# Performance work log

Hardware: AMD Instinct MI355X
Metric: run time of the kernel (lower is better)

## Reference

```python
import jax, jax.numpy as jnp
import numpy as np
import math

D_MODEL = 1024
HEADS = 16
D_K = D_MODEL // HEADS
BATCH = 4
SEQ = 1024


def setup_inputs() -> dict:
    key = jax.random.key(0)
    ks = jax.random.split(key, 12)
    s = 1.0 / math.sqrt(D_MODEL)
    inp = {
        "q": jax.random.normal(ks[0], (BATCH, SEQ, D_MODEL), jnp.float32),
        "k": jax.random.normal(ks[1], (BATCH, SEQ, D_MODEL), jnp.float32),
        "v": jax.random.normal(ks[2], (BATCH, SEQ, D_MODEL), jnp.float32),
        # causal mask, broadcastable over (batch, heads)
        "mask": jnp.tril(jnp.ones((SEQ, SEQ), jnp.bool_))[None, None, :, :],
        "Wq": jax.random.normal(ks[3], (D_MODEL, D_MODEL), jnp.float32) * s,
        "bq": jax.random.normal(ks[4], (D_MODEL,), jnp.float32) * 0.01,
        "Wk": jax.random.normal(ks[5], (D_MODEL, D_MODEL), jnp.float32) * s,
        "bk": jax.random.normal(ks[6], (D_MODEL,), jnp.float32) * 0.01,
        "Wv": jax.random.normal(ks[7], (D_MODEL, D_MODEL), jnp.float32) * s,
        "bv": jax.random.normal(ks[8], (D_MODEL,), jnp.float32) * 0.01,
        "Wo": jax.random.normal(ks[9], (D_MODEL, D_MODEL), jnp.float32) * s,
        "bo": jax.random.normal(ks[10], (D_MODEL,), jnp.float32) * 0.01,
    }
    return inp


def reference(q, k, v, mask, Wq, bq, Wk, bk, Wv, bv, Wo, bo):
    B, S, _ = q.shape
    # projections (torch Linear: x @ W.T + b; here W stored as [in, out])
    def proj(x, W, b):
        return (x @ W + b).reshape(B, -1, HEADS, D_K).transpose(0, 2, 1, 3)

    Q = proj(q, Wq, bq)  # [B, H, S, Dk]
    K = proj(k, Wk, bk)
    V = proj(v, Wv, bv)

    scores = jnp.einsum("bhqd,bhkd->bhqk", Q, K) / math.sqrt(D_K)
    scores = jnp.where(mask, scores, jnp.float32(-1e9))
    attn = jax.nn.softmax(scores, axis=-1)  # dropout p=0.0 -> identity
    x = jnp.einsum("bhqk,bhkd->bhqd", attn, V)
    x = x.transpose(0, 2, 1, 3).reshape(B, S, D_MODEL)
    return x @ Wo + bo
```

## Files before the change

kernel.cpp:

```cpp
#include <hip/hip_runtime.h>
#include <math.h>

typedef __bf16 bf16_t;
typedef bf16_t bf16x8 __attribute__((ext_vector_type(8)));
typedef bf16_t bf16x4 __attribute__((ext_vector_type(4)));
typedef float  floatx4 __attribute__((ext_vector_type(4)));
typedef unsigned int u32;

#define MFMA_BF16(a, b, c) __builtin_amdgcn_mfma_f32_16x16x32_bf16((a), (b), (c), 0, 0, 0)

static constexpr int DMODEL = 1024;
static constexpr int NHEAD  = 16;
static constexpr int HDIM   = 64;
static constexpr int NBATCH = 4;
static constexpr int SEQLEN = 1024;
static constexpr int NTOK   = NBATCH * SEQLEN;

typedef __attribute__((address_space(3))) void       as3_void;
typedef __attribute__((address_space(1))) const void as1_cvoid;

__device__ __forceinline__ void gload16(const void* g, void* l) {
    __builtin_amdgcn_global_load_lds((as1_cvoid*)g, (as3_void*)l, 16, 0, 0);
}

__device__ __forceinline__ bf16x8 load_cvt8(const float* __restrict__ p) {
    floatx4 a = *(const floatx4*)p;
    floatx4 b = *(const floatx4*)(p + 4);
    bf16x8 r;
    r[0] = (bf16_t)a[0]; r[1] = (bf16_t)a[1]; r[2] = (bf16_t)a[2]; r[3] = (bf16_t)a[3];
    r[4] = (bf16_t)b[0]; r[5] = (bf16_t)b[1]; r[6] = (bf16_t)b[2]; r[7] = (bf16_t)b[3];
    return r;
}

__global__ __launch_bounds__(256) void prep(
    const float* __restrict__ W0, const float* __restrict__ W1,
    const float* __restrict__ W2, const float* __restrict__ W3,
    const float* __restrict__ q, const float* __restrict__ k, const float* __restrict__ v,
    bf16_t* __restrict__ Wt, bf16_t* __restrict__ Xr)
{
    __shared__ float tile[32][33];
    const int z = blockIdx.z;
    if (z < 4) {
        const float* W = (z == 0) ? W0 : (z == 1) ? W1 : (z == 2) ? W2 : W3;
        bf16_t* O = Wt + (size_t)z * DMODEL * DMODEL;
        const int tx = threadIdx.x & 31, ty = threadIdx.x >> 5;
        const int r0 = blockIdx.x * 32, c0 = blockIdx.y * 32;
#pragma unroll
        for (int i = 0; i < 32; i += 8)
            tile[ty + i][tx] = W[(size_t)(r0 + ty + i) * DMODEL + c0 + tx];
        __syncthreads();
#pragma unroll
        for (int i = 0; i < 32; i += 8)
            O[(size_t)(c0 + ty + i) * DMODEL + r0 + tx] = (bf16_t)tile[tx][ty + i];
    } else {
        const float* src = (z == 4) ? q : (z == 5) ? k : v;
        bf16_t* dst = Xr + (size_t)(z - 4) * ((size_t)NTOK * DMODEL);
        size_t i = (((size_t)blockIdx.y * 32 + blockIdx.x) * 256 + threadIdx.x) * 16;
        *(bf16x8*)(dst + i)     = load_cvt8(src + i);
        *(bf16x8*)(dst + i + 8) = load_cvt8(src + i + 8);
    }
}

__global__ __launch_bounds__(256) void transpose_w(
    const float* __restrict__ W0, const float* __restrict__ W1,
    const float* __restrict__ W2, const float* __restrict__ W3,
    bf16_t* __restrict__ out)
{
    __shared__ float tile[32][33];
    const float* W = (blockIdx.z == 0) ? W0 : (blockIdx.z == 1) ? W1
                   : (blockIdx.z == 2) ? W2 : W3;
    bf16_t* O = out + (size_t)blockIdx.z * DMODEL * DMODEL;
    int tx = threadIdx.x, ty = threadIdx.y;
    int r0 = blockIdx.x * 32, c0 = blockIdx.y * 32;
#pragma unroll
    for (int i = 0; i < 32; i += 8)
        tile[ty + i][tx] = W[(size_t)(r0 + ty + i) * DMODEL + c0 + tx];
    __syncthreads();
#pragma unroll
    for (int i = 0; i < 32; i += 8)
        O[(size_t)(c0 + ty + i) * DMODEL + r0 + tx] = (bf16_t)tile[tx][ty + i];
}
__global__ __launch_bounds__(256) void cvt_bf16(
    const float* __restrict__ src, bf16_t* __restrict__ dst)
{
    size_t i = ((size_t)blockIdx.x * 256 + threadIdx.x) * 8;
    *(bf16x8*)(dst + i) = load_cvt8(src + i);
}

__global__ __launch_bounds__(256) void gemm_qkv(
    const bf16_t* __restrict__ Xb, size_t astride, int mode0,
    const bf16_t* __restrict__ Wt,
    const float* __restrict__ bq, const float* __restrict__ bk, const float* __restrict__ bv,
    bf16_t* __restrict__ Qh, bf16_t* __restrict__ Kh, bf16_t* __restrict__ Vt)
{
    const int mode = mode0 + blockIdx.z;
    const bf16_t* A = Xb + astride * (size_t)blockIdx.z;
    const bf16_t* B = Wt + (size_t)mode * DMODEL * DMODEL;
    const float* bias = (mode == 0) ? bq : (mode == 1) ? bk : bv;
    bf16_t* out       = (mode == 0) ? Qh : (mode == 1) ? Kh : Vt;

    __shared__ __align__(16) bf16_t lA[2][128 * 32];
    __shared__ __align__(16) bf16_t lB[2][128 * 32];

    const int wave = threadIdx.x >> 6, lane = threadIdx.x & 63;
    const int quad = lane >> 4, l15 = lane & 15;
    const int wm = wave >> 1, wn = wave & 1;
    const int row0 = blockIdx.x * 128, col0 = blockIdx.y * 128;
    const int srow = lane >> 2, scol = (lane & 3) * 8;

    const floatx4 zero = {0.f, 0.f, 0.f, 0.f};
    floatx4 acc[4][4];
#pragma unroll
    for (int mt = 0; mt < 4; mt++)
#pragma unroll
        for (int nt = 0; nt < 4; nt++) acc[mt][nt] = zero;

#pragma unroll
    for (int j = 0; j < 2; j++) {
        const int seg = j * 4 + wave;
        gload16(A + (size_t)(row0 + seg * 16 + srow) * DMODEL + scol, lA[0] + seg * 512);
        gload16(B + (size_t)(col0 + seg * 16 + srow) * DMODEL + scol, lB[0] + seg * 512);
    }

    for (int it = 0; it < 32; it++) {
        __syncthreads();
        const int cur = it & 1;
        if (it + 1 < 32) {
            const int k1 = (it + 1) * 32;
            const int nb = cur ^ 1;
#pragma unroll
            for (int j = 0; j < 2; j++) {
                const int seg = j * 4 + wave;
                gload16(A + (size_t)(row0 + seg * 16 + srow) * DMODEL + k1 + scol, lA[nb] + seg * 512);
                gload16(B + (size_t)(col0 + seg * 16 + srow) * DMODEL + k1 + scol, lB[nb] + seg * 512);
            }
        }
        bf16x8 aF[4], bF[4];
#pragma unroll
        for (int t = 0; t < 4; t++) {
            aF[t] = *(const bf16x8*)(lA[cur] + (wm * 64 + t * 16 + l15) * 32 + quad * 8);
            bF[t] = *(const bf16x8*)(lB[cur] + (wn * 64 + t * 16 + l15) * 32 + quad * 8);
        }
#pragma unroll
        for (int mt = 0; mt < 4; mt++)
#pragma unroll
            for (int nt = 0; nt < 4; nt++)
                acc[mt][nt] = MFMA_BF16(aF[mt], bF[nt], acc[mt][nt]);
    }

#pragma unroll
    for (int nt = 0; nt < 4; nt++) {
        const int gn = col0 + wn * 64 + nt * 16 + l15;
        const float bb = bias[gn];
        const int hh = gn >> 6, dd = gn & 63;
#pragma unroll
        for (int mt = 0; mt < 4; mt++) {
#pragma unroll
            for (int r = 0; r < 4; r++) {
                const int tok = row0 + wm * 64 + mt * 16 + quad * 4 + r;
                const int b = tok >> 10, s = tok & 1023;
                float vv = acc[mt][nt][r] + bb;
                size_t addr;
                if (mode == 2) {
                    addr = ((size_t)((b * NHEAD + hh) * HDIM + dd)) * SEQLEN + s;
                } else {
                    if (mode == 0) vv *= 0.125f;
                    addr = ((size_t)((b * NHEAD + hh) * SEQLEN + s)) * HDIM + dd;
                }
                out[addr] = (bf16_t)vv;
            }
        }
    }
}

__global__ __launch_bounds__(256) void gemm_o(
    const bf16_t* __restrict__ Xa, const bf16_t* __restrict__ Wt,
    const float* __restrict__ bias, float* __restrict__ out)
{
    __shared__ __align__(16) bf16_t lA[2][64 * 32];
    __shared__ __align__(16) bf16_t lB[2][128 * 32];

    const int wave = threadIdx.x >> 6, lane = threadIdx.x & 63;
    const int quad = lane >> 4, l15 = lane & 15;
    const int wm = wave & 1, wn = wave >> 1;
    const int row0 = blockIdx.x * 64, col0 = blockIdx.y * 128;
    const int srow = lane >> 2, scol = (lane & 3) * 8;

    const floatx4 zero = {0.f, 0.f, 0.f, 0.f};
    floatx4 acc[2][4];
#pragma unroll
    for (int mt = 0; mt < 2; mt++)
#pragma unroll
        for (int nt = 0; nt < 4; nt++) acc[mt][nt] = zero;

    gload16(Xa + (size_t)(row0 + wave * 16 + srow) * DMODEL + scol, lA[0] + wave * 512);
#pragma unroll
    for (int j = 0; j < 2; j++) {
        const int seg = wave * 2 + j;
        gload16(Wt + (size_t)(col0 + seg * 16 + srow) * DMODEL + scol, lB[0] + seg * 512);
    }

    for (int it = 0; it < 32; it++) {
        __syncthreads();
        const int cur = it & 1;
        if (it + 1 < 32) {
            const int k1 = (it + 1) * 32;
            const int nb = cur ^ 1;
            gload16(Xa + (size_t)(row0 + wave * 16 + srow) * DMODEL + k1 + scol, lA[nb] + wave * 512);
#pragma unroll
            for (int j = 0; j < 2; j++) {
                const int seg = wave * 2 + j;
                gload16(Wt + (size_t)(col0 + seg * 16 + srow) * DMODEL + k1 + scol, lB[nb] + seg * 512);
            }
        }
        bf16x8 aF[2], bF[4];
#pragma unroll
        for (int t = 0; t < 2; t++)
            aF[t] = *(const bf16x8*)(lA[cur] + (wm * 32 + t * 16 + l15) * 32 + quad * 8);
#pragma unroll
        for (int t = 0; t < 4; t++)
            bF[t] = *(const bf16x8*)(lB[cur] + (wn * 64 + t * 16 + l15) * 32 + quad * 8);
#pragma unroll
        for (int mt = 0; mt < 2; mt++)
#pragma unroll
            for (int nt = 0; nt < 4; nt++)
                acc[mt][nt] = MFMA_BF16(aF[mt], bF[nt], acc[mt][nt]);
    }

#pragma unroll
    for (int nt = 0; nt < 4; nt++) {
        const int gn = col0 + wn * 64 + nt * 16 + l15;
        const float bb = bias[gn];
#pragma unroll
        for (int mt = 0; mt < 2; mt++) {
#pragma unroll
            for (int r = 0; r < 4; r++) {
                const int tok = row0 + wm * 32 + mt * 16 + quad * 4 + r;
                out[(size_t)tok * DMODEL + gn] = acc[mt][nt][r] + bb;
            }
        }
    }
}

#define SOFTMAX_PV(S0x, S1x, qbase, qrow, lacc, oacc) do {                             \
    const bool nomask = (kb + 31 <= (qbase));                                          \
    float ps = 0.f;                                                                    \
    union { bf16_t hh2[8]; u32 u[4]; } pk;                                             \
    _Pragma("unroll") for (int r = 0; r < 4; r++) {                                    \
        const int key0 = kb + quad * 4 + r;                                            \
        float s0 = (nomask || key0 <= (qrow))      ? S0x[r] : -1e30f;                  \
        float s1 = (nomask || key0 + 16 <= (qrow)) ? S1x[r] : -1e30f;                  \
        float e0 = __expf(s0), e1 = __expf(s1);                                        \
        ps += e0 + e1;                                                                 \
        pk.hh2[r] = (bf16_t)e0; pk.hh2[4 + r] = (bf16_t)e1;                            \
    }                                                                                  \
    lacc += ps;                                                                        \
    u32 a0 = __shfl(pk.u[0], srcA), a1 = __shfl(pk.u[1], srcA);                        \
    u32 a2 = __shfl(pk.u[0], srcB), a3 = __shfl(pk.u[1], srcB);                        \
    u32 b0 = __shfl(pk.u[2], srcA), b1 = __shfl(pk.u[3], srcA);                        \
    u32 b2 = __shfl(pk.u[2], srcB), b3 = __shfl(pk.u[3], srcB);                        \
    union { u32 u[4]; bf16x8 v; } bP;                                                  \
    bP.u[0] = hiP ? b0 : a0; bP.u[1] = hiP ? b1 : a1;                                  \
    bP.u[2] = hiP ? b2 : a2; bP.u[3] = hiP ? b3 : a3;                                  \
    _Pragma("unroll") for (int dt = 0; dt < 4; dt++)                                   \
        oacc[dt] = MFMA_BF16(Vv[dt], bP.v, oacc[dt]);                                  \
} while (0)

__global__ __launch_bounds__(256, 4) void attn(
    const bf16_t* __restrict__ Qh, const bf16_t* __restrict__ Kh,
    const bf16_t* __restrict__ Vt, bf16_t* __restrict__ X)
{
    __shared__ __align__(8) float comb[2][64][34];
    const int wave = threadIdx.x >> 6, lane = threadIdx.x & 63;
    const int quad = lane >> 4, l15 = lane & 15;
    const int L = blockIdx.x;
    const int bh = (L & 7) * 8 + ((L >> 3) & 7);
    const int t  = L >> 6;
    const int b = bh >> 4, h = bh & 15;

    const int qbaseA = 16 * t, qbaseB = 1008 - 16 * t;
    const int qrowA = qbaseA + l15, qrowB = qbaseB + l15;
    const int nkA = t / 2 + 1, nkB = 32 - t / 2;

    const bf16_t* Qp = Qh + (size_t)bh * SEQLEN * HDIM;
    const bf16_t* Kp = Kh + (size_t)bh * SEQLEN * HDIM;
    const bf16_t* Vp = Vt + (size_t)bh * HDIM * SEQLEN;

    bf16x8 bQA[2], bQB[2];
#pragma unroll
    for (int c = 0; c < 2; c++) {
        bQA[c] = *(const bf16x8*)(Qp + (size_t)qrowA * HDIM + c * 32 + quad * 8);
        bQB[c] = *(const bf16x8*)(Qp + (size_t)qrowB * HDIM + c * 32 + quad * 8);
    }

    const floatx4 zero = {0.f, 0.f, 0.f, 0.f};
    float lA_ = 0.f, lB_ = 0.f;
    floatx4 oA[4], oB[4];
#pragma unroll
    for (int dt = 0; dt < 4; dt++) { oA[dt] = zero; oB[dt] = zero; }

    const int srcA = ((quad & 1) ? 32 : 0) + l15;
    const int srcB = srcA + 16;
    const bool hiP = (quad >= 2);

    for (int kc = wave; kc < nkB; kc += 4) {
        const int kb = kc * 32;
        bf16x8 K0[2], K1[2], Vv[4];
#pragma unroll
        for (int c = 0; c < 2; c++) {
            K0[c] = *(const bf16x8*)(Kp + (size_t)(kb + l15) * HDIM + c * 32 + quad * 8);
            K1[c] = *(const bf16x8*)(Kp + (size_t)(kb + 16 + l15) * HDIM + c * 32 + quad * 8);
        }
#pragma unroll
        for (int dt = 0; dt < 4; dt++)
            Vv[dt] = *(const bf16x8*)(Vp + (size_t)(dt * 16 + l15) * SEQLEN + kb + quad * 8);

        const bool doA = (kc < nkA);
        floatx4 S0B = zero, S1B = zero, S0A = zero, S1A = zero;
#pragma unroll
        for (int c = 0; c < 2; c++) {
            S0B = MFMA_BF16(K0[c], bQB[c], S0B);
            S1B = MFMA_BF16(K1[c], bQB[c], S1B);
        }
        if (doA) {
#pragma unroll
            for (int c = 0; c < 2; c++) {
                S0A = MFMA_BF16(K0[c], bQA[c], S0A);
                S1A = MFMA_BF16(K1[c], bQA[c], S1A);
            }
        }
        SOFTMAX_PV(S0B, S1B, qbaseB, qrowB, lB_, oB);
        if (doA) { SOFTMAX_PV(S0A, S1A, qbaseA, qrowA, lA_, oA); }
    }

    auto publish = [&](int slot) {
        float2* d2 = (float2*)&comb[slot][lane][0];
#pragma unroll
        for (int dt = 0; dt < 4; dt++) {
            d2[2 * dt]     = make_float2(oA[dt][0], oA[dt][1]);
            d2[2 * dt + 1] = make_float2(oA[dt][2], oA[dt][3]);
            d2[8 + 2 * dt]     = make_float2(oB[dt][0], oB[dt][1]);
            d2[8 + 2 * dt + 1] = make_float2(oB[dt][2], oB[dt][3]);
        }
        d2[16] = make_float2(lA_, lB_);
    };
    auto accum = [&](int slot) {
        const float2* s2 = (const float2*)&comb[slot][lane][0];
#pragma unroll
        for (int dt = 0; dt < 4; dt++) {
            float2 x0 = s2[2 * dt], x1 = s2[2 * dt + 1];
            float2 y0 = s2[8 + 2 * dt], y1 = s2[8 + 2 * dt + 1];
            oA[dt][0] += x0.x; oA[dt][1] += x0.y; oA[dt][2] += x1.x; oA[dt][3] += x1.y;
            oB[dt][0] += y0.x; oB[dt][1] += y0.y; oB[dt][2] += y1.x; oB[dt][3] += y1.y;
        }
        float2 lp = s2[16];
        lA_ += lp.x; lB_ += lp.y;
    };

    if (wave & 1) publish(wave >> 1);
    __syncthreads();
    if (!(wave & 1)) accum(wave >> 1);
    __syncthreads();
    if (wave == 2) publish(0);
    __syncthreads();
    if (wave == 0) {
        accum(0);

        lA_ += __shfl_xor(lA_, 16); lA_ += __shfl_xor(lA_, 32);
        lB_ += __shfl_xor(lB_, 16); lB_ += __shfl_xor(lB_, 32);

        const float invA = 1.f / lA_, invB = 1.f / lB_;
#pragma unroll
        for (int dt = 0; dt < 4; dt++) {
            bf16x4 va, vb;
#pragma unroll
            for (int r = 0; r < 4; r++) {
                va[r] = (bf16_t)(oA[dt][r] * invA);
                vb[r] = (bf16_t)(oB[dt][r] * invB);
            }
            const size_t cofs = (size_t)h * HDIM + dt * 16 + quad * 4;
            *(bf16x4*)(&X[((size_t)(b * SEQLEN + qrowA)) * DMODEL + cofs]) = va;
            *(bf16x4*)(&X[((size_t)(b * SEQLEN + qrowB)) * DMODEL + cofs]) = vb;
        }
    }
}

extern "C" void kernel_launch(void* const* d_in, const int* in_sizes, int n_in,
                              void* d_out, int out_size, void* d_ws, size_t ws_size,
                              hipStream_t stream)
{
    const float* q  = (const float*)d_in[0];
    const float* k  = (const float*)d_in[1];
    const float* v  = (const float*)d_in[2];
    const float* Wq = (const float*)d_in[4];
    const float* bq = (const float*)d_in[5];
    const float* Wk = (const float*)d_in[6];
    const float* bk = (const float*)d_in[7];
    const float* Wv = (const float*)d_in[8];
    const float* bv = (const float*)d_in[9];
    const float* Wo = (const float*)d_in[10];
    const float* bo = (const float*)d_in[11];
    float* out = (float*)d_out;

    char* ws = (char*)d_ws;
    const size_t MB = 1ull << 20;
    const size_t NELEM = (size_t)NTOK * DMODEL;
    bf16_t* Wt = (bf16_t*)ws;
    bf16_t* Qh = (bf16_t*)(ws + 8 * MB);
    bf16_t* Kh = (bf16_t*)(ws + 16 * MB);
    bf16_t* Vt = (bf16_t*)(ws + 24 * MB);
    bf16_t* Xr = (bf16_t*)(ws + 32 * MB);

    if (ws_size >= 56 * MB) {
        prep<<<dim3(32, 32, 7), dim3(256), 0, stream>>>(Wq, Wk, Wv, Wo, q, k, v, Wt, Xr);
        gemm_qkv<<<dim3(32, 8, 3), dim3(256), 0, stream>>>(
            Xr, NELEM, 0, Wt, bq, bk, bv, Qh, Kh, Vt);
    } else {
        transpose_w<<<dim3(32, 32, 4), dim3(32, 8), 0, stream>>>(Wq, Wk, Wv, Wo, Wt);
        const float* qkv_in[3] = {q, k, v};
        for (int m = 0; m < 3; m++) {
            cvt_bf16<<<dim3(2048), dim3(256), 0, stream>>>(qkv_in[m], Xr);
            gemm_qkv<<<dim3(32, 8, 1), dim3(256), 0, stream>>>(
                Xr, 0, m, Wt, bq, bk, bv, Qh, Kh, Vt);
        }
    }

    bf16_t* Xa = Xr;
    attn<<<dim3(2048), dim3(256), 0, stream>>>(Qh, Kh, Vt, Xa);
    gemm_o<<<dim3(64, 8), dim3(256), 0, stream>>>(
        Xa, Wt + 3 * (size_t)DMODEL * DMODEL, bo, out);
}
```

Measured before the change: 238.0 us.

## Double-buffer K/V loads in attention loop, use exp2 with folded log2e scale

Restructures the attention key loop into a two-stage software pipeline: the next K/V chunk is loaded into registers while the current one is computed, with sched_barriers keeping the loads ahead of the compute. Folds log2(e) into the Q scale so softmax can call a native exp2, and splits the fully unmasked path from the masked one to skip per-element mask checks. Raises MFMA wave priority and lowers launch bounds occupancy from 4 to 2 to make room for the extra registers held by the double buffers.

```diff
diff --git a/kernel.cpp b/kernel.cpp
--- a/kernel.cpp
+++ b/kernel.cpp
@@ -8,6 +8,12 @@
 typedef unsigned int u32;
 
 #define MFMA_BF16(a, b, c) __builtin_amdgcn_mfma_f32_16x16x32_bf16((a), (b), (c), 0, 0, 0)
+
+#if __has_builtin(__builtin_amdgcn_exp2f)
+#define EXP2F(x) __builtin_amdgcn_exp2f(x)
+#else
+#define EXP2F(x) exp2f(x)
+#endif
 
 static constexpr int DMODEL = 1024;
 static constexpr int NHEAD  = 16;
@@ -164,7 +170,7 @@
                 if (mode == 2) {
                     addr = ((size_t)((b * NHEAD + hh) * HDIM + dd)) * SEQLEN + s;
                 } else {
-                    if (mode == 0) vv *= 0.125f;
+                    if (mode == 0) vv *= 0.1803368801111204f;
                     addr = ((size_t)((b * NHEAD + hh) * SEQLEN + s)) * HDIM + dd;
                 }
                 out[addr] = (bf16_t)vv;
@@ -242,19 +248,7 @@
     }
 }
 
-#define SOFTMAX_PV(S0x, S1x, qbase, qrow, lacc, oacc) do {                             \
-    const bool nomask = (kb + 31 <= (qbase));                                          \
-    float ps = 0.f;                                                                    \
-    union { bf16_t hh2[8]; u32 u[4]; } pk;                                             \
-    _Pragma("unroll") for (int r = 0; r < 4; r++) {                                    \
-        const int key0 = kb + quad * 4 + r;                                            \
-        float s0 = (nomask || key0 <= (qrow))      ? S0x[r] : -1e30f;                  \
-        float s1 = (nomask || key0 + 16 <= (qrow)) ? S1x[r] : -1e30f;                  \
-        float e0 = __expf(s0), e1 = __expf(s1);                                        \
-        ps += e0 + e1;                                                                 \
-        pk.hh2[r] = (bf16_t)e0; pk.hh2[4 + r] = (bf16_t)e1;                            \
-    }                                                                                  \
-    lacc += ps;                                                                        \
+#define SHUF_PV(pk, Vv, oacc) do {                                                     \
     u32 a0 = __shfl(pk.u[0], srcA), a1 = __shfl(pk.u[1], srcA);                        \
     u32 a2 = __shfl(pk.u[0], srcB), a3 = __shfl(pk.u[1], srcB);                        \
     u32 b0 = __shfl(pk.u[2], srcA), b1 = __shfl(pk.u[3], srcA);                        \
@@ -262,11 +256,75 @@
     union { u32 u[4]; bf16x8 v; } bP;                                                  \
     bP.u[0] = hiP ? b0 : a0; bP.u[1] = hiP ? b1 : a1;                                  \
     bP.u[2] = hiP ? b2 : a2; bP.u[3] = hiP ? b3 : a3;                                  \
+    __builtin_amdgcn_s_setprio(1);                                                     \
     _Pragma("unroll") for (int dt = 0; dt < 4; dt++)                                   \
         oacc[dt] = MFMA_BF16(Vv[dt], bP.v, oacc[dt]);                                  \
+    __builtin_amdgcn_s_setprio(0);                                                     \
 } while (0)
 
-__global__ __launch_bounds__(256, 4) void attn(
+#define SOFTMAX_PV_FAST(S0x, S1x, Vv, lacc, oacc) do {                                 \
+    float ps = 0.f;                                                                    \
+    union { bf16_t hh2[8]; u32 u[4]; } pk;                                             \
+    _Pragma("unroll") for (int r = 0; r < 4; r++) {                                    \
+        float e0 = EXP2F(S0x[r]), e1 = EXP2F(S1x[r]);                                  \
+        ps += e0 + e1;                                                                 \
+        pk.hh2[r] = (bf16_t)e0; pk.hh2[4 + r] = (bf16_t)e1;                            \
+    }                                                                                  \
+    lacc += ps;                                                                        \
+    SHUF_PV(pk, Vv, oacc);                                                             \
+} while (0)
+
+#define SOFTMAX_PV_MASK(S0x, S1x, Vv, kbv, qrow, lacc, oacc) do {                      \
+    float ps = 0.f;                                                                    \
+    union { bf16_t hh2[8]; u32 u[4]; } pk;                                             \
+    _Pragma("unroll") for (int r = 0; r < 4; r++) {                                    \
+        const int key0 = (kbv) + quad * 4 + r;                                         \
+        float s0 = (key0 <= (qrow))      ? S0x[r] : -1e30f;                            \
+        float s1 = (key0 + 16 <= (qrow)) ? S1x[r] : -1e30f;                            \
+        float e0 = EXP2F(s0), e1 = EXP2F(s1);                                          \
+        ps += e0 + e1;                                                                 \
+        pk.hh2[r] = (bf16_t)e0; pk.hh2[4 + r] = (bf16_t)e1;                            \
+    }                                                                                  \
+    lacc += ps;                                                                        \
+    SHUF_PV(pk, Vv, oacc);                                                             \
+} while (0)
+
+#define LOAD_KV(K0v, K1v, Vv, kbv) do {                                                \
+    _Pragma("unroll") for (int c = 0; c < 2; c++) {                                    \
+        K0v[c] = *(const bf16x8*)(Kp + (size_t)((kbv) + l15) * HDIM + c * 32 + quad * 8);      \
+        K1v[c] = *(const bf16x8*)(Kp + (size_t)((kbv) + 16 + l15) * HDIM + c * 32 + quad * 8); \
+    }                                                                                  \
+    _Pragma("unroll") for (int dt = 0; dt < 4; dt++)                                   \
+        Vv[dt] = *(const bf16x8*)(Vp + (size_t)(dt * 16 + l15) * SEQLEN + (kbv) + quad * 8);   \
+} while (0)
+
+#define COMPUTE(K0v, K1v, Vv, kcv) do {                                                \
+    const int kb_ = (kcv) * 32;                                                        \
+    const bool doA_ = (kcv) < nkA;                                                     \
+    floatx4 S0B = zero, S1B = zero, S0A = zero, S1A = zero;                            \
+    __builtin_amdgcn_s_setprio(1);                                                     \
+    _Pragma("unroll") for (int c = 0; c < 2; c++) {                                    \
+        S0B = MFMA_BF16(K0v[c], bQB[c], S0B);                                          \
+        S1B = MFMA_BF16(K1v[c], bQB[c], S1B);                                          \
+    }                                                                                  \
+    __builtin_amdgcn_s_setprio(0);                                                     \
+    if (doA_) {                                                                        \
+        __builtin_amdgcn_s_setprio(1);                                                 \
+        _Pragma("unroll") for (int c = 0; c < 2; c++) {                                \
+            S0A = MFMA_BF16(K0v[c], bQA[c], S0A);                                      \
+            S1A = MFMA_BF16(K1v[c], bQA[c], S1A);                                      \
+        }                                                                              \
+        __builtin_amdgcn_s_setprio(0);                                                 \
+    }                                                                                  \
+    if (kb_ + 31 <= qbaseB) { SOFTMAX_PV_FAST(S0B, S1B, Vv, lB_, oB); }                \
+    else                    { SOFTMAX_PV_MASK(S0B, S1B, Vv, kb_, qrowB, lB_, oB); }    \
+    if (doA_) {                                                                        \
+        if (kb_ + 31 <= qbaseA) { SOFTMAX_PV_FAST(S0A, S1A, Vv, lA_, oA); }            \
+        else                    { SOFTMAX_PV_MASK(S0A, S1A, Vv, kb_, qrowA, lA_, oA); }\
+    }                                                                                  \
+} while (0)
+
+__global__ __launch_bounds__(256, 2) void attn(
     const bf16_t* __restrict__ Qh, const bf16_t* __restrict__ Kh,
     const bf16_t* __restrict__ Vt, bf16_t* __restrict__ X)
 {
@@ -303,35 +361,22 @@
     const int srcB = srcA + 16;
     const bool hiP = (quad >= 2);
 
-    for (int kc = wave; kc < nkB; kc += 4) {
-        const int kb = kc * 32;
-        bf16x8 K0[2], K1[2], Vv[4];
-#pragma unroll
-        for (int c = 0; c < 2; c++) {
-            K0[c] = *(const bf16x8*)(Kp + (size_t)(kb + l15) * HDIM + c * 32 + quad * 8);
-            K1[c] = *(const bf16x8*)(Kp + (size_t)(kb + 16 + l15) * HDIM + c * 32 + quad * 8);
-        }
-#pragma unroll
-        for (int dt = 0; dt < 4; dt++)
-            Vv[dt] = *(const bf16x8*)(Vp + (size_t)(dt * 16 + l15) * SEQLEN + kb + quad * 8);
-
-        const bool doA = (kc < nkA);
-        floatx4 S0B = zero, S1B = zero, S0A = zero, S1A = zero;
-#pragma unroll
-        for (int c = 0; c < 2; c++) {
-            S0B = MFMA_BF16(K0[c], bQB[c], S0B);
-            S1B = MFMA_BF16(K1[c], bQB[c], S1B);
-        }
-        if (doA) {
-#pragma unroll
-            for (int c = 0; c < 2; c++) {
-                S0A = MFMA_BF16(K0[c], bQA[c], S0A);
-                S1A = MFMA_BF16(K1[c], bQA[c], S1A);
-            }
-        }
-        SOFTMAX_PV(S0B, S1B, qbaseB, qrowB, lB_, oB);
-        if (doA) { SOFTMAX_PV(S0A, S1A, qbaseA, qrowA, lA_, oA); }
-    }
+    bf16x8 K0x[2], K1x[2], Vx[4];
+    bf16x8 K0y[2], K1y[2], Vy[4];
+    int kc = wave;
+    LOAD_KV(K0x, K1x, Vx, kc * 32);
+    __builtin_amdgcn_sched_barrier(0);
+    for (; kc + 4 < nkB; kc += 8) {
+        LOAD_KV(K0y, K1y, Vy, (kc + 4) * 32);
+        __builtin_amdgcn_sched_barrier(0);
+        COMPUTE(K0x, K1x, Vx, kc);
+        if (kc + 8 < nkB) {
+            LOAD_KV(K0x, K1x, Vx, (kc + 8) * 32);
+            __builtin_amdgcn_sched_barrier(0);
+        }
+        COMPUTE(K0y, K1y, Vy, kc + 4);
+    }
+    if (kc < nkB) COMPUTE(K0x, K1x, Vx, kc);
 
     auto publish = [&](int slot) {
         float2* d2 = (float2*)&comb[slot][lane][0];
```

After: 237.4 us. About the same (-0.3%).
